# Performance work log

Measured on AMD Instinct MI355X. Metric: run time of the kernel, lower is better.

## Reference

```python
import jax, jax.numpy as jnp
import numpy as np

B, L, DIM, H = 2, 2048, 1024, 16
HD = DIM // H  # 64
EPS = 1e-6
ROPE_THETA = 10000.0


def _rmsnorm(x, scale):
    # mean of squares in float32 as in torch (dtype=torch.float32)
    ms = jnp.mean(jnp.square(x.astype(jnp.float32)), axis=-1, keepdims=True)
    inv = jax.lax.rsqrt(ms + EPS).astype(x.dtype)
    return x * inv * scale.astype(x.dtype)


def _rope_cos_sin(seq_len, head_dim, dtype):
    inv_freq = 1.0 / (ROPE_THETA ** (jnp.arange(0, head_dim, 2, dtype=jnp.float32) / head_dim))
    ang = jnp.arange(seq_len, dtype=jnp.float32)[:, None] * inv_freq[None, :]  # [L, HD/2]
    cos = jnp.cos(ang)[:, None, :].astype(dtype)  # [L,1,HD/2] broadcast over heads
    sin = jnp.sin(ang)[:, None, :].astype(dtype)
    return cos, sin


def _rope_apply(x, cos, sin):
    # x: [B,L,H,HD]; rotate-half formulation
    x1, x2 = jnp.split(x, 2, axis=-1)
    return jnp.concatenate([x1 * cos - x2 * sin, x2 * cos + x1 * sin], axis=-1)


def setup_inputs() -> dict:
    key = jax.random.key(0)
    k1, k2, k3 = jax.random.split(key, 3)
    x = jax.random.normal(k1, (B, L, DIM), dtype=jnp.float32)
    Wqkv = jax.random.normal(k2, (DIM, 3 * DIM), dtype=jnp.float32) * (DIM ** -0.5)
    Wproj = jax.random.normal(k3, (DIM, DIM), dtype=jnp.float32) * (DIM ** -0.5)
    q_scale = jnp.ones((HD,), dtype=jnp.float32)
    k_scale = jnp.ones((HD,), dtype=jnp.float32)
    bproj = jnp.zeros((DIM,), dtype=jnp.float32)
    return {"x": x, "Wqkv": Wqkv, "q_scale": q_scale, "k_scale": k_scale,
            "Wproj": Wproj, "bproj": bproj}


def reference(x, Wqkv, q_scale, k_scale, Wproj, bproj):
    b, l, c = x.shape
    qkv = x @ Wqkv  # [B,L,3*DIM]
    qkv = qkv.reshape(b, l, 3, H, HD)
    q, k, v = qkv[:, :, 0], qkv[:, :, 1], qkv[:, :, 2]  # each [B,L,H,HD]
    q = _rmsnorm(q, q_scale)
    k = _rmsnorm(k, k_scale)
    cos, sin = _rope_cos_sin(l, HD, x.dtype)
    q = _rope_apply(q, cos, sin)
    k = _rope_apply(k, cos, sin)
    scale = HD ** -0.5
    scores = jnp.einsum('blhd,bmhd->bhlm', q, k) * scale  # [B,H,L,L]
    p = jax.nn.softmax(scores, axis=-1)
    o = jnp.einsum('bhlm,bmhd->blhd', p, v).reshape(b, l, c)
    return o @ Wproj + bproj
```

## Files before the change

kernel.cpp:

```cpp
#include <hip/hip_runtime.h>
#include <hip/hip_bf16.h>
#include <cstdint>

#define B_   2
#define L_   2048
#define DIM_ 1024
#define H_   16
#define HD_  64
#define M_   (B_ * L_)
#define N3_  (3 * DIM_)

typedef unsigned short ushort_t;
typedef __bf16 bf16x8 __attribute__((ext_vector_type(8)));
typedef float  f32x4  __attribute__((ext_vector_type(4)));
typedef float  f32x16 __attribute__((ext_vector_type(16)));
typedef unsigned u32x2_t __attribute__((ext_vector_type(2)));

__device__ __forceinline__ unsigned short f2b(float f) {
  return __builtin_bit_cast(unsigned short, (__bf16)f);
}
__device__ __forceinline__ float b2f(unsigned short s) {
  unsigned u = ((unsigned)s) << 16;
  return __builtin_bit_cast(float, u);
}
__device__ __forceinline__ float fmax3(float a, float b, float c) {
  return fmaxf(fmaxf(a, b), c);
}

__device__ __forceinline__ void plswap(unsigned &a, unsigned &b) {
#if defined(__has_builtin) && __has_builtin(__builtin_amdgcn_permlane32_swap)
  u32x2_t r = __builtin_amdgcn_permlane32_swap(a, b, false, false);
  a = r[0]; b = r[1];
#else
  unsigned sa = (unsigned)__shfl_xor((int)a, 32);
  unsigned sb = (unsigned)__shfl_xor((int)b, 32);
  bool hi = (threadIdx.x & 32) != 0;
  unsigned na = hi ? sb : a;
  unsigned nb = hi ? b : sa;
  a = na; b = nb;
#endif
}

typedef const __attribute__((address_space(1))) void* as1cp;
typedef __attribute__((address_space(3))) void* as3p;
__device__ __forceinline__ void gload_lds16(const void* g, void* l) {
  __builtin_amdgcn_global_load_lds((as1cp)g, (as3p)l, 16, 0, 0);
}

__global__ __launch_bounds__(256)
void preproc(const float* __restrict__ x, ushort_t* __restrict__ xb,
             const float* __restrict__ Wqkv, ushort_t* __restrict__ WqkvT,
             const float* __restrict__ Wproj, ushort_t* __restrict__ WprojT,
             float* __restrict__ cosT, float* __restrict__ sinT) {
  __shared__ float tile[64][65];
  const int blk = blockIdx.x;
  const int t = threadIdx.x;
  if (blk < 4096) {
    int i = blk * 256 + t;
    float4 v = *(const float4*)&x[(size_t)i * 4];
    ushort4 o;
    o.x = f2b(v.x); o.y = f2b(v.y); o.z = f2b(v.z); o.w = f2b(v.w);
    *(ushort4*)&xb[(size_t)i * 4] = o;
  } else if (blk < 5120) {
    const float* in;
    ushort_t* out;
    int C, bi;
    if (blk < 4864) { in = Wqkv; out = WqkvT; C = 3072; bi = blk - 4096; }
    else            { in = Wproj; out = WprojT; C = 1024; bi = blk - 4864; }
    const int nbx = C >> 6;
    const int bx = bi % nbx, by = bi / nbx;
    const int r0 = by * 64, c0 = bx * 64;
    const int R = 1024;
#pragma unroll
    for (int p = 0; p < 4; ++p) {
      int r = (t >> 4) + p * 16;
      int c = (t & 15) * 4;
      float4 v = *(const float4*)&in[(size_t)(r0 + r) * C + (c0 + c)];
      tile[r][c + 0] = v.x; tile[r][c + 1] = v.y;
      tile[r][c + 2] = v.z; tile[r][c + 3] = v.w;
    }
    __syncthreads();
#pragma unroll
    for (int p = 0; p < 4; ++p) {
      int cc = (t >> 4) + p * 16;
      int r  = (t & 15) * 4;
      ushort4 o;
      o.x = f2b(tile[r + 0][cc]); o.y = f2b(tile[r + 1][cc]);
      o.z = f2b(tile[r + 2][cc]); o.w = f2b(tile[r + 3][cc]);
      *(ushort4*)&out[(size_t)(c0 + cc) * R + (r0 + r)] = o;
    }
  } else {
    int idx = (blk - 5120) * 256 + t;
    int l = idx >> 5, d = idx & 31;
    float inv_freq = expf(-((float)(2 * d) / 64.f) * logf(10000.f));
    float ang = (float)l * inv_freq;
    cosT[idx] = cosf(ang);
    sinT[idx] = sinf(ang);
  }
}

template <int MODE>
__global__ __launch_bounds__(256)
void gemm_bt(const ushort_t* __restrict__ A, const ushort_t* __restrict__ BT,
             void* __restrict__ Cout, ushort_t* __restrict__ vtout,
             const float* __restrict__ bias, int M, int N, int K, int ldc,
             const float* __restrict__ qsc_, const float* __restrict__ ksc_,
             const float* __restrict__ cosT, const float* __restrict__ sinT) {
  __shared__ ushort_t As[128 * 32];
  __shared__ ushort_t Bs[128 * 32];
  const int lane = threadIdx.x & 63;
  const int wid  = threadIdx.x >> 6;
  const int wm = wid >> 1, wn = wid & 1;
  const int m0 = blockIdx.y * 128, n0 = blockIdx.x * 128;
  const int ro = lane & 15, kg = lane >> 4;

  f32x4 acc[4][4] = {};

  for (int k0 = 0; k0 < K; k0 += 32) {
    const int cb = wid * 128;
#pragma unroll
    for (int j = 0; j < 2; ++j) {
      int c = cb + j * 64 + lane;
      gload_lds16(A + (size_t)(m0 + (c >> 2)) * K + k0 + (c & 3) * 8,
                  &As[(cb + j * 64) * 8]);
    }
#pragma unroll
    for (int j = 0; j < 2; ++j) {
      int c = cb + j * 64 + lane;
      gload_lds16(BT + (size_t)(n0 + (c >> 2)) * K + k0 + (c & 3) * 8,
                  &Bs[(cb + j * 64) * 8]);
    }
    __syncthreads();
    bf16x8 af[4], bfr[4];
#pragma unroll
    for (int i = 0; i < 4; ++i)
      af[i] = *(const bf16x8*)&As[(wm * 64 + i * 16 + ro) * 32 + kg * 8];
#pragma unroll
    for (int i = 0; i < 4; ++i)
      bfr[i] = *(const bf16x8*)&Bs[(wn * 64 + i * 16 + ro) * 32 + kg * 8];
#pragma unroll
    for (int i = 0; i < 4; ++i)
#pragma unroll
      for (int j = 0; j < 4; ++j)
        acc[i][j] = __builtin_amdgcn_mfma_f32_16x16x32_bf16(af[i], bfr[j],
                                                            acc[i][j], 0, 0, 0);
    __syncthreads();
  }

  if (MODE == 0) {
    if (n0 < 2048) {
      const int ic = (n0 >= 1024);
      const float* scp = ic ? ksc_ : qsc_;
      const float qsc = ic ? 1.f : 0.125f * 1.44269504088896341f;
      float sc[4];
#pragma unroll
      for (int j = 0; j < 4; ++j) sc[j] = scp[j * 16 + ro];
#pragma unroll
      for (int i = 0; i < 4; ++i)
#pragma unroll
        for (int r = 0; r < 4; ++r) {
          int row = m0 + wm * 64 + i * 16 + kg * 4 + r;
          int l = row & (L_ - 1);
          float x0 = acc[i][0][r], x1 = acc[i][1][r];
          float x2 = acc[i][2][r], x3 = acc[i][3][r];
          float ss = x0 * x0 + x1 * x1 + x2 * x2 + x3 * x3;
          ss += __shfl_xor(ss, 1); ss += __shfl_xor(ss, 2);
          ss += __shfl_xor(ss, 4); ss += __shfl_xor(ss, 8);
          float inv = rsqrtf(ss * (1.f / 64.f) + 1e-6f);
          x0 *= inv * sc[0]; x1 *= inv * sc[1];
          x2 *= inv * sc[2]; x3 *= inv * sc[3];
          float cv0 = cosT[l * 32 + ro],      sv0 = sinT[l * 32 + ro];
          float cv1 = cosT[l * 32 + 16 + ro], sv1 = sinT[l * 32 + 16 + ro];
          float o0 = (x0 * cv0 - x2 * sv0) * qsc;
          float o1 = (x1 * cv1 - x3 * sv1) * qsc;
          float o2 = (x2 * cv0 + x0 * sv0) * qsc;
          float o3 = (x3 * cv1 + x1 * sv1) * qsc;
          ushort_t* cp = (ushort_t*)Cout + (size_t)row * ldc + n0 + wn * 64 + ro;
          cp[0]  = f2b(o0);
          cp[16] = f2b(o1);
          cp[32] = f2b(o2);
          cp[48] = f2b(o3);
        }
    } else {
#pragma unroll
      for (int i = 0; i < 4; ++i) {
        int rowb = m0 + wm * 64 + i * 16 + kg * 4;
        int bb = rowb >> 11, l = rowb & (L_ - 1);
#pragma unroll
        for (int j = 0; j < 4; ++j) {
          int dg = (n0 - 2048) + wn * 64 + j * 16 + ro;
          ushort4 o;
          o.x = f2b(acc[i][j][0]); o.y = f2b(acc[i][j][1]);
          o.z = f2b(acc[i][j][2]); o.w = f2b(acc[i][j][3]);
          *(ushort4*)&vtout[((size_t)bb * DIM_ + dg) * L_ + l] = o;
        }
      }
    }
  } else {
#pragma unroll
    for (int i = 0; i < 4; ++i)
#pragma unroll
      for (int r = 0; r < 4; ++r) {
        int row = m0 + wm * 64 + i * 16 + kg * 4 + r;
#pragma unroll
        for (int j = 0; j < 4; ++j) {
          int col = n0 + wn * 64 + j * 16 + ro;
          ((float*)Cout)[(size_t)row * ldc + col] = acc[i][j][r] + bias[col];
        }
      }
  }
}

template <int SPLIT>
__global__ __launch_bounds__(256, 3)
void flash_attn(const ushort_t* __restrict__ qk, const ushort_t* __restrict__ vt,
                ushort_t* __restrict__ O, ushort_t* __restrict__ Opart,
                float* __restrict__ Ml) {
  const int qt = blockIdx.x, h = blockIdx.y;
  const int b  = SPLIT ? (int)(blockIdx.z >> 1) : (int)blockIdx.z;
  const int ks = SPLIT ? (int)(blockIdx.z & 1) : 0;
  const int ktBeg = SPLIT ? ks * (L_ / 128) : 0;
  const int ktEnd = SPLIT ? ktBeg + (L_ / 128) : (L_ / 64);
  const int lane = threadIdx.x & 63, wid = threadIdx.x >> 6;
  const int lq = lane & 31;
  const int hi = lane >> 5;
  const int q0 = qt * 128;
  const size_t tok0 = (size_t)b * L_;
  const ushort_t* qb = qk + tok0 * 2048 + h * HD_;
  const ushort_t* kb = qb + DIM_;
  const ushort_t* vb = vt + ((size_t)b * DIM_ + h * HD_) * L_;

  __shared__ ushort_t Ks[2][4096];
  __shared__ ushort_t Vs[2][4096];

  const int srow0 = wid * 16 + (lane >> 3);
  const int sc    = (lane & 7) ^ (srow0 & 7);
  const ushort_t* kst = kb + (size_t)(ktBeg * 64 + srow0) * 2048 + sc * 8;
  const ushort_t* vst = vb + (size_t)srow0 * L_ + ktBeg * 64 + sc * 8;
  auto STAGE = [&](int bufi) {
    gload_lds16(kst,            &Ks[bufi][wid * 1024]);
    gload_lds16(kst + 8 * 2048, &Ks[bufi][wid * 1024 + 512]);
    gload_lds16(vst,            &Vs[bufi][wid * 1024]);
    gload_lds16(vst + 8 * L_,   &Vs[bufi][wid * 1024 + 512]);
    kst += 64 * 2048;
    vst += 64;
  };

  bf16x8 qf[4];
  {
    const ushort_t* gp = qb + (size_t)(q0 + wid * 32 + lq) * 2048;
#pragma unroll
    for (int s = 0; s < 4; ++s)
      qf[s] = *(const bf16x8*)(gp + s * 16 + hi * 8);
  }

  bf16x8 onesv;
#pragma unroll
  for (int i = 0; i < 8; ++i) onesv[i] = (__bf16)1.0f;

  int chs[4];
#pragma unroll
  for (int s = 0; s < 4; ++s) chs[s] = ((2 * s + hi) ^ (lq & 7)) * 8;

  f32x16 oaccT[2] = {};
  f32x16 laccv = {};
  float mrow = 0.f;

  STAGE(0);
  __syncthreads();

  auto TILE = [&](int bi, bool more) {
    if (more) STAGE(bi ^ 1);
    const ushort_t* kb0 = &Ks[bi][lq * 64];
    const ushort_t* vb0 = &Vs[bi][lq * 64];

    f32x16 st0, st1;
#pragma unroll
    for (int i = 0; i < 16; ++i) { st0[i] = -mrow; st1[i] = -mrow; }
    __builtin_amdgcn_s_setprio(1);
#pragma unroll
    for (int s = 0; s < 4; ++s) {
      bf16x8 kf0 = *(const bf16x8*)(kb0 + chs[s]);
      bf16x8 kf1 = *(const bf16x8*)(kb0 + 2048 + chs[s]);
      st0 = __builtin_amdgcn_mfma_f32_32x32x16_bf16(kf0, qf[s], st0, 0, 0, 0);
      st1 = __builtin_amdgcn_mfma_f32_32x32x16_bf16(kf1, qf[s], st1, 0, 0, 0);
    }
    __builtin_amdgcn_s_setprio(0);

    float a0 = fmax3(st0[0],  st0[1],  st0[2]);
    float a1 = fmax3(st0[3],  st0[4],  st0[5]);
    float a2 = fmax3(st0[6],  st0[7],  st0[8]);
    float a3 = fmax3(st0[9],  st0[10], st0[11]);
    float a4 = fmax3(st0[12], st0[13], st0[14]);
    float a5 = fmax3(st0[15], st1[0],  st1[1]);
    float a6 = fmax3(st1[2],  st1[3],  st1[4]);
    float a7 = fmax3(st1[5],  st1[6],  st1[7]);
    float a8 = fmax3(st1[8],  st1[9],  st1[10]);
    float a9 = fmax3(st1[11], st1[12], st1[13]);
    float aa = fmaxf(st1[14], st1[15]);
    float c0 = fmax3(a0, a1, a2);
    float c1 = fmax3(a3, a4, a5);
    float c2 = fmax3(a6, a7, a8);
    float c3 = fmax3(a9, aa, c0);
    float pm = fmax3(c1, c2, c3);
    pm = fmaxf(pm, __shfl_xor(pm, 32));

    if (__any(pm > 8.f)) {
      float d = fmaxf(pm, 0.f);
      float alpha = __builtin_amdgcn_exp2f(-d);
      mrow += d;
      laccv[0] *= alpha;
#pragma unroll
      for (int dt = 0; dt < 2; ++dt)
#pragma unroll
        for (int r = 0; r < 16; ++r) oaccT[dt][r] *= alpha;
#pragma unroll
      for (int i = 0; i < 16; ++i) { st0[i] -= d; st1[i] -= d; }
    }

    unsigned pk0[8], pk1[8];
#pragma unroll
    for (int p = 0; p < 8; ++p) {
      float e0 = __builtin_amdgcn_exp2f(st0[2 * p]);
      float e1 = __builtin_amdgcn_exp2f(st0[2 * p + 1]);
      pk0[p] = (unsigned)f2b(e0) | ((unsigned)f2b(e1) << 16);
      float f0 = __builtin_amdgcn_exp2f(st1[2 * p]);
      float f1 = __builtin_amdgcn_exp2f(st1[2 * p + 1]);
      pk1[p] = (unsigned)f2b(f0) | ((unsigned)f2b(f1) << 16);
    }

    __builtin_amdgcn_s_setprio(1);
#pragma unroll
    for (int t = 0; t < 2; ++t)
#pragma unroll
      for (int blk = 0; blk < 2; ++blk) {
        unsigned w0 = (t == 0) ? pk0[4 * blk + 0] : pk1[4 * blk + 0];
        unsigned w1 = (t == 0) ? pk0[4 * blk + 1] : pk1[4 * blk + 1];
        unsigned w2 = (t == 0) ? pk0[4 * blk + 2] : pk1[4 * blk + 2];
        unsigned w3 = (t == 0) ? pk0[4 * blk + 3] : pk1[4 * blk + 3];
        plswap(w0, w2);
        plswap(w1, w3);
        uint4 bw; bw.x = w0; bw.y = w1; bw.z = w2; bw.w = w3;
        bf16x8 pf = __builtin_bit_cast(bf16x8, bw);
        const int sg = 2 * t + blk;
        laccv = __builtin_amdgcn_mfma_f32_32x32x16_bf16(onesv, pf, laccv, 0, 0, 0);
#pragma unroll
        for (int dt = 0; dt < 2; ++dt) {
          bf16x8 vf = *(const bf16x8*)(vb0 + dt * 2048 + chs[sg]);
          oaccT[dt] = __builtin_amdgcn_mfma_f32_32x32x16_bf16(vf, pf,
                                                              oaccT[dt], 0, 0, 0);
        }
      }
    __builtin_amdgcn_s_setprio(0);

    __syncthreads();
  };

  const int NT = ktEnd - ktBeg;
  for (int it = 0; it < NT; it += 2) {
    TILE(0, it + 1 < NT);
    TILE(1, it + 2 < NT);
  }

  const float lrow = laccv[0];
  const float linv = 1.f / lrow;
  const int tok = (int)tok0 + q0 + wid * 32 + lq;
  ushort_t* obp = (SPLIT ? Opart + (size_t)ks * M_ * DIM_ : O)
                  + (size_t)tok * DIM_ + h * HD_;
#pragma unroll
  for (int dt = 0; dt < 2; ++dt)
#pragma unroll
    for (int g4 = 0; g4 < 4; ++g4) {
      int d0 = dt * 32 + g4 * 8 + hi * 4;
      ushort4 o4;
      o4.x = f2b(oaccT[dt][4 * g4 + 0] * linv);
      o4.y = f2b(oaccT[dt][4 * g4 + 1] * linv);
      o4.z = f2b(oaccT[dt][4 * g4 + 2] * linv);
      o4.w = f2b(oaccT[dt][4 * g4 + 3] * linv);
      *(ushort4*)(obp + d0) = o4;
    }
  if (SPLIT && hi == 0) {
    float2 ml; ml.x = mrow; ml.y = lrow;
    *(float2*)&Ml[(((size_t)ks * M_ + tok) * H_ + h) * 2] = ml;
  }
}

__global__ __launch_bounds__(256)
void attn_combine(const ushort_t* __restrict__ Opart, const float* __restrict__ Ml,
                  ushort_t* __restrict__ O) {
  int idx = blockIdx.x * 256 + threadIdx.x;
  int c   = idx & 127;
  int tok = idx >> 7;
  int h   = c >> 3;
  float2 ml0 = *(const float2*)&Ml[(((size_t)0 * M_ + tok) * H_ + h) * 2];
  float2 ml1 = *(const float2*)&Ml[(((size_t)1 * M_ + tok) * H_ + h) * 2];
  float mM = fmaxf(ml0.x, ml1.x);
  float w0 = ml0.y * __builtin_amdgcn_exp2f(ml0.x - mM);
  float w1 = ml1.y * __builtin_amdgcn_exp2f(ml1.x - mM);
  float inv = 1.f / (w0 + w1);
  w0 *= inv; w1 *= inv;
  size_t off = (size_t)tok * DIM_ + c * 8;
  uint4 a = *(const uint4*)&Opart[off];
  uint4 d = *(const uint4*)&Opart[(size_t)M_ * DIM_ + off];
  auto mix = [&](unsigned ua, unsigned ud) -> unsigned {
    float a0 = b2f((unsigned short)(ua & 0xffff)), a1 = b2f((unsigned short)(ua >> 16));
    float d0 = b2f((unsigned short)(ud & 0xffff)), d1 = b2f((unsigned short)(ud >> 16));
    unsigned r0 = f2b(a0 * w0 + d0 * w1), r1 = f2b(a1 * w0 + d1 * w1);
    return r0 | (r1 << 16);
  };
  uint4 o;
  o.x = mix(a.x, d.x); o.y = mix(a.y, d.y);
  o.z = mix(a.z, d.z); o.w = mix(a.w, d.w);
  *(uint4*)&O[off] = o;
}

extern "C" void kernel_launch(void* const* d_in, const int* in_sizes, int n_in,
                              void* d_out, int out_size, void* d_ws, size_t ws_size,
                              hipStream_t stream) {
  const float* x     = (const float*)d_in[0];
  const float* Wqkv  = (const float*)d_in[1];
  const float* qs    = (const float*)d_in[2];
  const float* ks    = (const float*)d_in[3];
  const float* Wproj = (const float*)d_in[4];
  const float* bproj = (const float*)d_in[5];
  float* out = (float*)d_out;

  char* ws = (char*)d_ws;
  ushort_t* xb     = (ushort_t*)(ws);
  ushort_t* WqkvT  = (ushort_t*)(ws + (size_t)(8u << 20));
  ushort_t* WprojT = (ushort_t*)(ws + (size_t)(14u << 20));
  ushort_t* qkb    = (ushort_t*)(ws + (size_t)(16u << 20));
  ushort_t* vtb    = (ushort_t*)(ws + (size_t)(32u << 20));
  float*    cosT   = (float*)(ws + (size_t)(40u << 20));
  float*    sinT   = (float*)(ws + (size_t)(40u << 20) + (256u << 10));
  ushort_t* ob     = (ushort_t*)(ws + (size_t)(41u << 20));
  ushort_t* Opart  = (ushort_t*)(ws + (size_t)(49u << 20));
  float*    Ml     = (float*)(ws + (size_t)(65u << 20));

  preproc<<<5376, 256, 0, stream>>>(x, xb, Wqkv, WqkvT, Wproj, WprojT,
                                    cosT, sinT);
  gemm_bt<0><<<dim3(24, 32), 256, 0, stream>>>(xb, WqkvT, qkb, vtb, nullptr,
                                               M_, N3_, DIM_, 2048,
                                               qs, ks, cosT, sinT);
  if (ws_size >= ((size_t)66u << 20)) {
    flash_attn<1><<<dim3(16, 16, 4), 256, 0, stream>>>(qkb, vtb, nullptr,
                                                       Opart, Ml);
    attn_combine<<<2048, 256, 0, stream>>>(Opart, Ml, ob);
  } else {
    flash_attn<0><<<dim3(16, 16, 2), 256, 0, stream>>>(qkb, vtb, ob,
                                                       nullptr, nullptr);
  }
  gemm_bt<1><<<dim3(8, 32), 256, 0, stream>>>(ob, WprojT, out, nullptr, bproj,
                                              M_, DIM_, DIM_, DIM_,
                                              nullptr, nullptr, nullptr, nullptr);
}
```

Before: 140.2 us.

## Rewrite QKV GEMM with 256x256 tiles, triple-buffered LDS and swizzle

Replaces the templated QKV GEMM with a dedicated kernel that uses 512 threads, 256x256 output tiles, a three-stage LDS ring buffer filled by async global-to-LDS loads, and an XOR-swizzled LDS layout to avoid bank conflicts. The aim is to overlap global loads with MFMA work, raise per-block data reuse, and cut the barrier count per K step. The RMSNorm/RoPE epilogue is kept. The trade-off is much higher register and LDS use (96 KB LDS, 32 accumulator tiles per wave) and only 192 blocks, which may underfill the GPU's compute units.

```diff
diff --git a/kernel.cpp b/kernel.cpp
--- a/kernel.cpp
+++ b/kernel.cpp
@@ -99,13 +99,143 @@
   }
 }
 
-template <int MODE>
+__global__ __launch_bounds__(512, 2)
+void gemm_qkv(const ushort_t* __restrict__ A, const ushort_t* __restrict__ BT,
+              ushort_t* __restrict__ Cqk, ushort_t* __restrict__ vtout,
+              const float* __restrict__ qsc_, const float* __restrict__ ksc_,
+              const float* __restrict__ cosT, const float* __restrict__ sinT) {
+  __shared__ ushort_t As[3][8192];
+  __shared__ ushort_t Bs[3][8192];
+  const int K = DIM_;
+  const int NT = K >> 5;
+  const int lane = threadIdx.x & 63;
+  const int wid  = threadIdx.x >> 6;
+  const int wm = wid >> 2, wn = wid & 3;
+  const int m0 = blockIdx.y * 256, n0 = blockIdx.x * 256;
+  const int ro = lane & 15, kg = lane >> 4;
+
+  const int srow  = lane >> 2;
+  const int schnk = (lane & 3) ^ ((lane >> 3) & 3);
+  const ushort_t* astA0 = A + (size_t)(m0 + (wid * 2 + 0) * 16 + srow) * K + schnk * 8;
+  const ushort_t* astA1 = A + (size_t)(m0 + (wid * 2 + 1) * 16 + srow) * K + schnk * 8;
+  const ushort_t* bstB0 = BT + (size_t)(n0 + (wid * 2 + 0) * 16 + srow) * K + schnk * 8;
+  const ushort_t* bstB1 = BT + (size_t)(n0 + (wid * 2 + 1) * 16 + srow) * K + schnk * 8;
+  const int awA0 = (wid * 2 + 0) * 512;
+  const int awA1 = (wid * 2 + 1) * 512;
+
+  auto STAGE = [&](int s2, int ko) {
+    gload_lds16(astA0 + ko, &As[s2][awA0]);
+    gload_lds16(astA1 + ko, &As[s2][awA1]);
+    gload_lds16(bstB0 + ko, &Bs[s2][awA0]);
+    gload_lds16(bstB1 + ko, &Bs[s2][awA1]);
+  };
+
+  const int ach = kg ^ ((ro >> 1) & 3);
+  const int aro = (wm * 128 + ro) * 32 + ach * 8;
+  const int bro = (wn * 64 + ro) * 32 + ach * 8;
+
+  f32x4 acc[8][4] = {};
+
+  STAGE(0, 0);
+  STAGE(1, 32);
+  asm volatile("s_waitcnt vmcnt(4)" ::: "memory");
+  __builtin_amdgcn_sched_barrier(0);
+  __builtin_amdgcn_s_barrier();
+  __builtin_amdgcn_sched_barrier(0);
+
+  int slot = 0, s2 = 2;
+  for (int t = 0; t < NT; ++t) {
+    if (t + 2 < NT) STAGE(s2, (t + 2) * 32);
+
+    const ushort_t* ab = &As[slot][aro];
+    const ushort_t* bb = &Bs[slot][bro];
+    bf16x8 bfr[4];
+#pragma unroll
+    for (int fn = 0; fn < 4; ++fn)
+      bfr[fn] = *(const bf16x8*)(bb + fn * 512);
+#pragma unroll
+    for (int q = 0; q < 4; ++q) {
+      bf16x8 a0 = *(const bf16x8*)(ab + (2 * q) * 512);
+      bf16x8 a1 = *(const bf16x8*)(ab + (2 * q + 1) * 512);
+      __builtin_amdgcn_s_setprio(1);
+#pragma unroll
+      for (int fn = 0; fn < 4; ++fn)
+        acc[2 * q][fn] = __builtin_amdgcn_mfma_f32_16x16x32_bf16(
+            a0, bfr[fn], acc[2 * q][fn], 0, 0, 0);
+#pragma unroll
+      for (int fn = 0; fn < 4; ++fn)
+        acc[2 * q + 1][fn] = __builtin_amdgcn_mfma_f32_16x16x32_bf16(
+            a1, bfr[fn], acc[2 * q + 1][fn], 0, 0, 0);
+      __builtin_amdgcn_s_setprio(0);
+    }
+
+    if (t + 2 < NT) {
+      asm volatile("s_waitcnt vmcnt(4)" ::: "memory");
+    } else {
+      asm volatile("s_waitcnt vmcnt(0)" ::: "memory");
+    }
+    __builtin_amdgcn_sched_barrier(0);
+    __builtin_amdgcn_s_barrier();
+    __builtin_amdgcn_sched_barrier(0);
+
+    slot = (slot == 2) ? 0 : slot + 1;
+    s2   = (s2 == 2) ? 0 : s2 + 1;
+  }
+
+  if (n0 < 2048) {
+    const int ic = (n0 >= 1024);
+    const float* scp = ic ? ksc_ : qsc_;
+    const float qsc = ic ? 1.f : 0.125f * 1.44269504088896341f;
+    float sc[4];
+#pragma unroll
+    for (int j = 0; j < 4; ++j) sc[j] = scp[j * 16 + ro];
+#pragma unroll
+    for (int fr = 0; fr < 8; ++fr)
+#pragma unroll
+      for (int r = 0; r < 4; ++r) {
+        int row = m0 + wm * 128 + fr * 16 + kg * 4 + r;
+        int l = row & (L_ - 1);
+        float x0 = acc[fr][0][r], x1 = acc[fr][1][r];
+        float x2 = acc[fr][2][r], x3 = acc[fr][3][r];
+        float ss = x0 * x0 + x1 * x1 + x2 * x2 + x3 * x3;
+        ss += __shfl_xor(ss, 1); ss += __shfl_xor(ss, 2);
+        ss += __shfl_xor(ss, 4); ss += __shfl_xor(ss, 8);
+        float inv = rsqrtf(ss * (1.f / 64.f) + 1e-6f);
+        x0 *= inv * sc[0]; x1 *= inv * sc[1];
+        x2 *= inv * sc[2]; x3 *= inv * sc[3];
+        float cv0 = cosT[l * 32 + ro],      sv0 = sinT[l * 32 + ro];
+        float cv1 = cosT[l * 32 + 16 + ro], sv1 = sinT[l * 32 + 16 + ro];
+        float o0 = (x0 * cv0 - x2 * sv0) * qsc;
+        float o1 = (x1 * cv1 - x3 * sv1) * qsc;
+        float o2 = (x2 * cv0 + x0 * sv0) * qsc;
+        float o3 = (x3 * cv1 + x1 * sv1) * qsc;
+        ushort_t* cp = Cqk + (size_t)row * 2048 + n0 + wn * 64 + ro;
+        cp[0]  = f2b(o0);
+        cp[16] = f2b(o1);
+        cp[32] = f2b(o2);
+        cp[48] = f2b(o3);
+      }
+  } else {
+#pragma unroll
+    for (int fr = 0; fr < 8; ++fr) {
+      int rowb = m0 + wm * 128 + fr * 16 + kg * 4;
+      int bb = rowb >> 11, l = rowb & (L_ - 1);
+#pragma unroll
+      for (int fn = 0; fn < 4; ++fn) {
+        int dg = (n0 - 2048) + wn * 64 + fn * 16 + ro;
+        ushort4 o;
+        o.x = f2b(acc[fr][fn][0]); o.y = f2b(acc[fr][fn][1]);
+        o.z = f2b(acc[fr][fn][2]); o.w = f2b(acc[fr][fn][3]);
+        *(ushort4*)&vtout[((size_t)bb * DIM_ + dg) * L_ + l] = o;
+      }
+    }
+  }
+}
+
 __global__ __launch_bounds__(256)
-void gemm_bt(const ushort_t* __restrict__ A, const ushort_t* __restrict__ BT,
-             void* __restrict__ Cout, ushort_t* __restrict__ vtout,
-             const float* __restrict__ bias, int M, int N, int K, int ldc,
-             const float* __restrict__ qsc_, const float* __restrict__ ksc_,
-             const float* __restrict__ cosT, const float* __restrict__ sinT) {
+void gemm_proj(const ushort_t* __restrict__ A, const ushort_t* __restrict__ BT,
+               float* __restrict__ Cout, const float* __restrict__ bias,
+               int M, int N, int K, int ldc) {
   __shared__ ushort_t As[128 * 32];
   __shared__ ushort_t Bs[128 * 32];
   const int lane = threadIdx.x & 63;
@@ -147,68 +277,17 @@
     __syncthreads();
   }
 
-  if (MODE == 0) {
-    if (n0 < 2048) {
-      const int ic = (n0 >= 1024);
-      const float* scp = ic ? ksc_ : qsc_;
-      const float qsc = ic ? 1.f : 0.125f * 1.44269504088896341f;
-      float sc[4];
-#pragma unroll
-      for (int j = 0; j < 4; ++j) sc[j] = scp[j * 16 + ro];
-#pragma unroll
-      for (int i = 0; i < 4; ++i)
-#pragma unroll
-        for (int r = 0; r < 4; ++r) {
-          int row = m0 + wm * 64 + i * 16 + kg * 4 + r;
-          int l = row & (L_ - 1);
-          float x0 = acc[i][0][r], x1 = acc[i][1][r];
-          float x2 = acc[i][2][r], x3 = acc[i][3][r];
-          float ss = x0 * x0 + x1 * x1 + x2 * x2 + x3 * x3;
-          ss += __shfl_xor(ss, 1); ss += __shfl_xor(ss, 2);
-          ss += __shfl_xor(ss, 4); ss += __shfl_xor(ss, 8);
-          float inv = rsqrtf(ss * (1.f / 64.f) + 1e-6f);
-          x0 *= inv * sc[0]; x1 *= inv * sc[1];
-          x2 *= inv * sc[2]; x3 *= inv * sc[3];
-          float cv0 = cosT[l * 32 + ro],      sv0 = sinT[l * 32 + ro];
-          float cv1 = cosT[l * 32 + 16 + ro], sv1 = sinT[l * 32 + 16 + ro];
-          float o0 = (x0 * cv0 - x2 * sv0) * qsc;
-          float o1 = (x1 * cv1 - x3 * sv1) * qsc;
-          float o2 = (x2 * cv0 + x0 * sv0) * qsc;
-          float o3 = (x3 * cv1 + x1 * sv1) * qsc;
-          ushort_t* cp = (ushort_t*)Cout + (size_t)row * ldc + n0 + wn * 64 + ro;
-          cp[0]  = f2b(o0);
-          cp[16] = f2b(o1);
-          cp[32] = f2b(o2);
-          cp[48] = f2b(o3);
-        }
-    } else {
-#pragma unroll
-      for (int i = 0; i < 4; ++i) {
-        int rowb = m0 + wm * 64 + i * 16 + kg * 4;
-        int bb = rowb >> 11, l = rowb & (L_ - 1);
-#pragma unroll
-        for (int j = 0; j < 4; ++j) {
-          int dg = (n0 - 2048) + wn * 64 + j * 16 + ro;
-          ushort4 o;
-          o.x = f2b(acc[i][j][0]); o.y = f2b(acc[i][j][1]);
-          o.z = f2b(acc[i][j][2]); o.w = f2b(acc[i][j][3]);
-          *(ushort4*)&vtout[((size_t)bb * DIM_ + dg) * L_ + l] = o;
-        }
+#pragma unroll
+  for (int i = 0; i < 4; ++i)
+#pragma unroll
+    for (int r = 0; r < 4; ++r) {
+      int row = m0 + wm * 64 + i * 16 + kg * 4 + r;
+#pragma unroll
+      for (int j = 0; j < 4; ++j) {
+        int col = n0 + wn * 64 + j * 16 + ro;
+        Cout[(size_t)row * ldc + col] = acc[i][j][r] + bias[col];
       }
     }
-  } else {
-#pragma unroll
-    for (int i = 0; i < 4; ++i)
-#pragma unroll
-      for (int r = 0; r < 4; ++r) {
-        int row = m0 + wm * 64 + i * 16 + kg * 4 + r;
-#pragma unroll
-        for (int j = 0; j < 4; ++j) {
-          int col = n0 + wn * 64 + j * 16 + ro;
-          ((float*)Cout)[(size_t)row * ldc + col] = acc[i][j][r] + bias[col];
-        }
-      }
-  }
 }
 
 template <int SPLIT>
@@ -439,9 +518,8 @@
 
   preproc<<<5376, 256, 0, stream>>>(x, xb, Wqkv, WqkvT, Wproj, WprojT,
                                     cosT, sinT);
-  gemm_bt<0><<<dim3(24, 32), 256, 0, stream>>>(xb, WqkvT, qkb, vtb, nullptr,
-                                               M_, N3_, DIM_, 2048,
-                                               qs, ks, cosT, sinT);
+  gemm_qkv<<<dim3(12, 16), 512, 0, stream>>>(xb, WqkvT, qkb, vtb,
+                                             qs, ks, cosT, sinT);
   if (ws_size >= ((size_t)66u << 20)) {
     flash_attn<1><<<dim3(16, 16, 4), 256, 0, stream>>>(qkb, vtb, nullptr,
                                                        Opart, Ml);
@@ -450,7 +528,6 @@
     flash_attn<0><<<dim3(16, 16, 2), 256, 0, stream>>>(qkb, vtb, ob,
                                                        nullptr, nullptr);
   }
-  gemm_bt<1><<<dim3(8, 32), 256, 0, stream>>>(ob, WprojT, out, nullptr, bproj,
-                                              M_, DIM_, DIM_, DIM_,
-                                              nullptr, nullptr, nullptr, nullptr);
-}
+  gemm_proj<<<dim3(8, 32), 256, 0, stream>>>(ob, WprojT, out, bproj,
+                                             M_, DIM_, DIM_, DIM_);
+}
```

Result: slower. 146.3 us (+4.4%).

## Fuse split-K attention combine into output projection GEMM A-tile load

Applied to the files above, without the earlier changes.

Removes the separate attn_combine kernel by having the projection GEMM read both partial attention outputs, blend them with log-sum-exp weights per head, and write the blended bf16 tile into shared memory itself. The A operand now goes through registers with software prefetch of the next k-slice instead of direct global-to-LDS loads. This saves one launch and one full round trip of the combined output through memory. In exchange the GEMM reads twice as much A data, recomputes the weights once per block, and does more ALU work inside its main loop.

```diff
diff --git a/kernel.cpp b/kernel.cpp
--- a/kernel.cpp
+++ b/kernel.cpp
@@ -99,13 +99,12 @@
   }
 }
 
-template <int MODE>
 __global__ __launch_bounds__(256)
-void gemm_bt(const ushort_t* __restrict__ A, const ushort_t* __restrict__ BT,
-             void* __restrict__ Cout, ushort_t* __restrict__ vtout,
-             const float* __restrict__ bias, int M, int N, int K, int ldc,
-             const float* __restrict__ qsc_, const float* __restrict__ ksc_,
-             const float* __restrict__ cosT, const float* __restrict__ sinT) {
+void gemm_qkv(const ushort_t* __restrict__ A, const ushort_t* __restrict__ BT,
+              ushort_t* __restrict__ Cqk, ushort_t* __restrict__ vtout,
+              const float* __restrict__ qsc_, const float* __restrict__ ksc_,
+              const float* __restrict__ cosT, const float* __restrict__ sinT) {
+  const int K = DIM_;
   __shared__ ushort_t As[128 * 32];
   __shared__ ushort_t Bs[128 * 32];
   const int lane = threadIdx.x & 63;
@@ -147,68 +146,181 @@
     __syncthreads();
   }
 
-  if (MODE == 0) {
-    if (n0 < 2048) {
-      const int ic = (n0 >= 1024);
-      const float* scp = ic ? ksc_ : qsc_;
-      const float qsc = ic ? 1.f : 0.125f * 1.44269504088896341f;
-      float sc[4];
-#pragma unroll
-      for (int j = 0; j < 4; ++j) sc[j] = scp[j * 16 + ro];
-#pragma unroll
-      for (int i = 0; i < 4; ++i)
-#pragma unroll
-        for (int r = 0; r < 4; ++r) {
-          int row = m0 + wm * 64 + i * 16 + kg * 4 + r;
-          int l = row & (L_ - 1);
-          float x0 = acc[i][0][r], x1 = acc[i][1][r];
-          float x2 = acc[i][2][r], x3 = acc[i][3][r];
-          float ss = x0 * x0 + x1 * x1 + x2 * x2 + x3 * x3;
-          ss += __shfl_xor(ss, 1); ss += __shfl_xor(ss, 2);
-          ss += __shfl_xor(ss, 4); ss += __shfl_xor(ss, 8);
-          float inv = rsqrtf(ss * (1.f / 64.f) + 1e-6f);
-          x0 *= inv * sc[0]; x1 *= inv * sc[1];
-          x2 *= inv * sc[2]; x3 *= inv * sc[3];
-          float cv0 = cosT[l * 32 + ro],      sv0 = sinT[l * 32 + ro];
-          float cv1 = cosT[l * 32 + 16 + ro], sv1 = sinT[l * 32 + 16 + ro];
-          float o0 = (x0 * cv0 - x2 * sv0) * qsc;
-          float o1 = (x1 * cv1 - x3 * sv1) * qsc;
-          float o2 = (x2 * cv0 + x0 * sv0) * qsc;
-          float o3 = (x3 * cv1 + x1 * sv1) * qsc;
-          ushort_t* cp = (ushort_t*)Cout + (size_t)row * ldc + n0 + wn * 64 + ro;
-          cp[0]  = f2b(o0);
-          cp[16] = f2b(o1);
-          cp[32] = f2b(o2);
-          cp[48] = f2b(o3);
+  if (n0 < 2048) {
+    const int ic = (n0 >= 1024);
+    const float* scp = ic ? ksc_ : qsc_;
+    const float qsc = ic ? 1.f : 0.125f * 1.44269504088896341f;
+    float sc[4];
+#pragma unroll
+    for (int j = 0; j < 4; ++j) sc[j] = scp[j * 16 + ro];
+#pragma unroll
+    for (int i = 0; i < 4; ++i)
+#pragma unroll
+      for (int r = 0; r < 4; ++r) {
+        int row = m0 + wm * 64 + i * 16 + kg * 4 + r;
+        int l = row & (L_ - 1);
+        float x0 = acc[i][0][r], x1 = acc[i][1][r];
+        float x2 = acc[i][2][r], x3 = acc[i][3][r];
+        float ss = x0 * x0 + x1 * x1 + x2 * x2 + x3 * x3;
+        ss += __shfl_xor(ss, 1); ss += __shfl_xor(ss, 2);
+        ss += __shfl_xor(ss, 4); ss += __shfl_xor(ss, 8);
+        float inv = rsqrtf(ss * (1.f / 64.f) + 1e-6f);
+        x0 *= inv * sc[0]; x1 *= inv * sc[1];
+        x2 *= inv * sc[2]; x3 *= inv * sc[3];
+        float cv0 = cosT[l * 32 + ro],      sv0 = sinT[l * 32 + ro];
+        float cv1 = cosT[l * 32 + 16 + ro], sv1 = sinT[l * 32 + 16 + ro];
+        float o0 = (x0 * cv0 - x2 * sv0) * qsc;
+        float o1 = (x1 * cv1 - x3 * sv1) * qsc;
+        float o2 = (x2 * cv0 + x0 * sv0) * qsc;
+        float o3 = (x3 * cv1 + x1 * sv1) * qsc;
+        ushort_t* cp = Cqk + (size_t)row * 2048 + n0 + wn * 64 + ro;
+        cp[0]  = f2b(o0);
+        cp[16] = f2b(o1);
+        cp[32] = f2b(o2);
+        cp[48] = f2b(o3);
+      }
+  } else {
+#pragma unroll
+    for (int i = 0; i < 4; ++i) {
+      int rowb = m0 + wm * 64 + i * 16 + kg * 4;
+      int bb = rowb >> 11, l = rowb & (L_ - 1);
+#pragma unroll
+      for (int j = 0; j < 4; ++j) {
+        int dg = (n0 - 2048) + wn * 64 + j * 16 + ro;
+        ushort4 o;
+        o.x = f2b(acc[i][j][0]); o.y = f2b(acc[i][j][1]);
+        o.z = f2b(acc[i][j][2]); o.w = f2b(acc[i][j][3]);
+        *(ushort4*)&vtout[((size_t)bb * DIM_ + dg) * L_ + l] = o;
+      }
+    }
+  }
+}
+
+template <int COMB>
+__global__ __launch_bounds__(256)
+void gemm_proj(const ushort_t* __restrict__ A, const float* __restrict__ Ml,
+               const ushort_t* __restrict__ BT, float* __restrict__ Cout,
+               const float* __restrict__ bias) {
+  const int K = DIM_;
+  __shared__ ushort_t As[128 * 32];
+  __shared__ ushort_t Bs[128 * 32];
+  const int lane = threadIdx.x & 63;
+  const int wid  = threadIdx.x >> 6;
+  const int wm = wid >> 1, wn = wid & 1;
+  const int m0 = blockIdx.y * 128, n0 = blockIdx.x * 128;
+  const int ro = lane & 15, kg = lane >> 4;
+
+  const int cb = wid * 128;
+  const int c0 = cb + lane, c1 = cb + 64 + lane;
+  const int row0 = m0 + (c0 >> 2), row1 = m0 + (c1 >> 2);
+  const int kch0 = (c0 & 3) * 8,  kch1 = (c1 & 3) * 8;
+
+  f32x4 acc[4][4] = {};
+
+  auto STAGEB = [&](int k0) {
+    gload_lds16(BT + (size_t)(n0 + (c0 >> 2)) * K + k0 + kch0, &Bs[cb * 8]);
+    gload_lds16(BT + (size_t)(n0 + (c1 >> 2)) * K + k0 + kch1, &Bs[(cb + 64) * 8]);
+  };
+  auto COMPUTE = [&]() {
+    bf16x8 af[4], bfr[4];
+#pragma unroll
+    for (int i = 0; i < 4; ++i)
+      af[i] = *(const bf16x8*)&As[(wm * 64 + i * 16 + ro) * 32 + kg * 8];
+#pragma unroll
+    for (int i = 0; i < 4; ++i)
+      bfr[i] = *(const bf16x8*)&Bs[(wn * 64 + i * 16 + ro) * 32 + kg * 8];
+#pragma unroll
+    for (int i = 0; i < 4; ++i)
+#pragma unroll
+      for (int j = 0; j < 4; ++j)
+        acc[i][j] = __builtin_amdgcn_mfma_f32_16x16x32_bf16(af[i], bfr[j],
+                                                            acc[i][j], 0, 0, 0);
+  };
+
+  if constexpr (COMB == 0) {
+    for (int k0 = 0; k0 < K; k0 += 32) {
+      gload_lds16(A + (size_t)row0 * K + k0 + kch0, &As[cb * 8]);
+      gload_lds16(A + (size_t)row1 * K + k0 + kch1, &As[(cb + 64) * 8]);
+      STAGEB(k0);
+      __syncthreads();
+      COMPUTE();
+      __syncthreads();
+    }
+  } else {
+    uint4 rae[2][2], rao[2][2];
+    auto LOADA = [&](int k0, uint4 (&ra)[2][2]) {
+      const ushort_t* p0 = A + (size_t)row0 * 1024 + k0 + kch0;
+      const ushort_t* p1 = A + (size_t)row1 * 1024 + k0 + kch1;
+      ra[0][0] = *(const uint4*)p0;
+      ra[0][1] = *(const uint4*)(p0 + (size_t)M_ * 1024);
+      ra[1][0] = *(const uint4*)p1;
+      ra[1][1] = *(const uint4*)(p1 + (size_t)M_ * 1024);
+    };
+    auto BLENDW = [&](const uint4 (&ra)[2][2], const float* w0, const float* w1) {
+#pragma unroll
+      for (int j = 0; j < 2; ++j) {
+        int c = j ? c1 : c0;
+        const unsigned* pa = (const unsigned*)&ra[j][0];
+        const unsigned* pb = (const unsigned*)&ra[j][1];
+        unsigned ow[4];
+#pragma unroll
+        for (int w = 0; w < 4; ++w) {
+          float a0 = b2f((unsigned short)(pa[w] & 0xffff));
+          float a1 = b2f((unsigned short)(pa[w] >> 16));
+          float d0 = b2f((unsigned short)(pb[w] & 0xffff));
+          float d1 = b2f((unsigned short)(pb[w] >> 16));
+          unsigned r0 = f2b(a0 * w0[j] + d0 * w1[j]);
+          unsigned r1 = f2b(a1 * w0[j] + d1 * w1[j]);
+          ow[w] = r0 | (r1 << 16);
         }
-    } else {
-#pragma unroll
-      for (int i = 0; i < 4; ++i) {
-        int rowb = m0 + wm * 64 + i * 16 + kg * 4;
-        int bb = rowb >> 11, l = rowb & (L_ - 1);
-#pragma unroll
-        for (int j = 0; j < 4; ++j) {
-          int dg = (n0 - 2048) + wn * 64 + j * 16 + ro;
-          ushort4 o;
-          o.x = f2b(acc[i][j][0]); o.y = f2b(acc[i][j][1]);
-          o.z = f2b(acc[i][j][2]); o.w = f2b(acc[i][j][3]);
-          *(ushort4*)&vtout[((size_t)bb * DIM_ + dg) * L_ + l] = o;
+        uint4 o; o.x = ow[0]; o.y = ow[1]; o.z = ow[2]; o.w = ow[3];
+        *(uint4*)&As[c * 8] = o;
+      }
+    };
+
+    LOADA(0, rae);
+    for (int k0 = 0; k0 < K; k0 += 64) {
+      float w0[2], w1[2];
+      {
+        const int h = k0 >> 6;
+#pragma unroll
+        for (int j = 0; j < 2; ++j) {
+          int tok = j ? row1 : row0;
+          float2 ml0 = *(const float2*)&Ml[((size_t)tok * H_ + h) * 2];
+          float2 ml1 = *(const float2*)&Ml[(((size_t)(M_ + tok)) * H_ + h) * 2];
+          float mM = fmaxf(ml0.x, ml1.x);
+          float a = ml0.y * __builtin_amdgcn_exp2f(ml0.x - mM);
+          float b = ml1.y * __builtin_amdgcn_exp2f(ml1.x - mM);
+          float inv = 1.f / (a + b);
+          w0[j] = a * inv; w1[j] = b * inv;
         }
       }
-    }
-  } else {
-#pragma unroll
-    for (int i = 0; i < 4; ++i)
-#pragma unroll
-      for (int r = 0; r < 4; ++r) {
-        int row = m0 + wm * 64 + i * 16 + kg * 4 + r;
-#pragma unroll
-        for (int j = 0; j < 4; ++j) {
-          int col = n0 + wn * 64 + j * 16 + ro;
-          ((float*)Cout)[(size_t)row * ldc + col] = acc[i][j][r] + bias[col];
-        }
+      STAGEB(k0);
+      LOADA(k0 + 32, rao);
+      BLENDW(rae, w0, w1);
+      __syncthreads();
+      COMPUTE();
+      __syncthreads();
+      STAGEB(k0 + 32);
+      if (k0 + 64 < K) LOADA(k0 + 64, rae);
+      BLENDW(rao, w0, w1);
+      __syncthreads();
+      COMPUTE();
+      __syncthreads();
+    }
+  }
+
+#pragma unroll
+  for (int i = 0; i < 4; ++i)
+#pragma unroll
+    for (int r = 0; r < 4; ++r) {
+      int row = m0 + wm * 64 + i * 16 + kg * 4 + r;
+#pragma unroll
+      for (int j = 0; j < 4; ++j) {
+        int col = n0 + wn * 64 + j * 16 + ro;
+        Cout[(size_t)row * DIM_ + col] = acc[i][j][r] + bias[col];
       }
-  }
+    }
 }
 
 template <int SPLIT>
@@ -385,35 +497,6 @@
   }
 }
 
-__global__ __launch_bounds__(256)
-void attn_combine(const ushort_t* __restrict__ Opart, const float* __restrict__ Ml,
-                  ushort_t* __restrict__ O) {
-  int idx = blockIdx.x * 256 + threadIdx.x;
-  int c   = idx & 127;
-  int tok = idx >> 7;
-  int h   = c >> 3;
-  float2 ml0 = *(const float2*)&Ml[(((size_t)0 * M_ + tok) * H_ + h) * 2];
-  float2 ml1 = *(const float2*)&Ml[(((size_t)1 * M_ + tok) * H_ + h) * 2];
-  float mM = fmaxf(ml0.x, ml1.x);
-  float w0 = ml0.y * __builtin_amdgcn_exp2f(ml0.x - mM);
-  float w1 = ml1.y * __builtin_amdgcn_exp2f(ml1.x - mM);
-  float inv = 1.f / (w0 + w1);
-  w0 *= inv; w1 *= inv;
-  size_t off = (size_t)tok * DIM_ + c * 8;
-  uint4 a = *(const uint4*)&Opart[off];
-  uint4 d = *(const uint4*)&Opart[(size_t)M_ * DIM_ + off];
-  auto mix = [&](unsigned ua, unsigned ud) -> unsigned {
-    float a0 = b2f((unsigned short)(ua & 0xffff)), a1 = b2f((unsigned short)(ua >> 16));
-    float d0 = b2f((unsigned short)(ud & 0xffff)), d1 = b2f((unsigned short)(ud >> 16));
-    unsigned r0 = f2b(a0 * w0 + d0 * w1), r1 = f2b(a1 * w0 + d1 * w1);
-    return r0 | (r1 << 16);
-  };
-  uint4 o;
-  o.x = mix(a.x, d.x); o.y = mix(a.y, d.y);
-  o.z = mix(a.z, d.z); o.w = mix(a.w, d.w);
-  *(uint4*)&O[off] = o;
-}
-
 extern "C" void kernel_launch(void* const* d_in, const int* in_sizes, int n_in,
                               void* d_out, int out_size, void* d_ws, size_t ws_size,
                               hipStream_t stream) {
@@ -439,18 +522,15 @@
 
   preproc<<<5376, 256, 0, stream>>>(x, xb, Wqkv, WqkvT, Wproj, WprojT,
                                     cosT, sinT);
-  gemm_bt<0><<<dim3(24, 32), 256, 0, stream>>>(xb, WqkvT, qkb, vtb, nullptr,
-                                               M_, N3_, DIM_, 2048,
-                                               qs, ks, cosT, sinT);
+  gemm_qkv<<<dim3(24, 32), 256, 0, stream>>>(xb, WqkvT, qkb, vtb,
+                                             qs, ks, cosT, sinT);
   if (ws_size >= ((size_t)66u << 20)) {
     flash_attn<1><<<dim3(16, 16, 4), 256, 0, stream>>>(qkb, vtb, nullptr,
                                                        Opart, Ml);
-    attn_combine<<<2048, 256, 0, stream>>>(Opart, Ml, ob);
+    gemm_proj<1><<<dim3(8, 32), 256, 0, stream>>>(Opart, Ml, WprojT, out, bproj);
   } else {
     flash_attn<0><<<dim3(16, 16, 2), 256, 0, stream>>>(qkb, vtb, ob,
                                                        nullptr, nullptr);
-  }
-  gemm_bt<1><<<dim3(8, 32), 256, 0, stream>>>(ob, WprojT, out, nullptr, bproj,
-                                              M_, DIM_, DIM_, DIM_,
-                                              nullptr, nullptr, nullptr, nullptr);
-}
+    gemm_proj<0><<<dim3(8, 32), 256, 0, stream>>>(ob, nullptr, WprojT, out, bproj);
+  }
+}
```

After: 154.0 us. 9.8% more time.
